# Performance work log

Measured on AMD Instinct MI355X. Metric: run time of the kernel, lower is better.

The kernel has to match this reference:

```python
import jax, jax.numpy as jnp
import numpy as np

N, M, NCAPS, NHID, ROUTIT = 50000, 16, 8, 16, 6
D = NCAPS * NHID  # 128


def _normalize(x, axis):
    # torch fn.normalize: x / max(||x||, eps)
    return x / jnp.maximum(jnp.linalg.norm(x, axis=axis, keepdims=True), 1e-12)


def _routing(x, nb, k, dd, max_iter, fc_w=None, fc_b=None):
    # x: [n, d], nb: [n*m] int indices into rows of x (n == zero pad row)
    if fc_w is not None:
        x = jax.nn.relu(x @ fc_w.T + fc_b)
    n = x.shape[0]
    d = k * dd
    m = nb.shape[0] // n
    xn = _normalize(x.reshape(n, k, dd), 2)          # [n,k,dd]
    zsrc = jnp.concatenate([xn.reshape(n, d), jnp.zeros((1, d), x.dtype)], axis=0)
    z = zsrc[nb].reshape(n, m, k, dd)                # gathered neighbors
    u = xn
    for it in range(max_iter):
        p = jax.nn.softmax(jnp.einsum('nmkd,nkd->nmk', z, u), axis=2)
        u = jnp.einsum('nmkd,nmk->nkd', z, p) + xn
        if it < max_iter - 1:
            u = _normalize(u, 2)
    return u.reshape(n, d)


def setup_inputs() -> dict:
    key = jax.random.key(0)
    k1, k2, k3 = jax.random.split(key, 3)
    x = jax.random.normal(k1, (N, D), dtype=jnp.float32)
    nb = jax.random.randint(k2, (N * M,), 0, N)
    fc1_w = jax.random.normal(k3, (D, D), dtype=jnp.float32) * (1.0 / np.sqrt(D))
    fc1_b = jnp.zeros((D,), dtype=jnp.float32)
    return {"x": x, "nb": nb, "fc1_w": fc1_w, "fc1_b": fc1_b}


def reference(x, nb, fc1_w, fc1_b):
    nb = nb.reshape(-1)
    # layer 0: inp_caps=None -> no fc; dropout is identity in eval mode
    h = jax.nn.relu(_routing(x, nb, NCAPS, NHID, ROUTIT))
    # layer 1: fc Linear(D, D) then relu inside routing
    h = jax.nn.relu(_routing(h, nb, NCAPS, NHID, ROUTIT, fc1_w, fc1_b))
    return h
```

## Files before the change

### kernel.cpp

```cpp
#include <hip/hip_runtime.h>
#include <math.h>

#define N_NODES 50000
#define M_NB 16
#define K_CAPS 8
#define DD 16
#define D_DIM 128
#define ROUTIT 6

template <int CTRL>
__device__ __forceinline__ float dpp_add(float x) {
    int t = __builtin_amdgcn_update_dpp(0, __float_as_int(x), CTRL, 0xF, 0xF, true);
    return x + __int_as_float(t);
}

__device__ __forceinline__ float xor8_add(float x) {
    float d;
    asm("s_nop 1\n\t"
        "v_add_f32_dpp %0, %1, %1 row_ror:8 row_mask:0xf bank_mask:0xf"
        : "=v"(d) : "v"(x));
    return d;
}

__device__ __forceinline__ float xor16_add(float x) {
#if __has_builtin(__builtin_amdgcn_permlane16_swap)
    unsigned xi = __float_as_uint(x);
    auto r = __builtin_amdgcn_permlane16_swap(xi, xi, false, false);
    return __uint_as_float(r[0]) + __uint_as_float(r[1]);
#else
    return x + __int_as_float(__builtin_amdgcn_ds_swizzle(__float_as_int(x), 0x401F));
#endif
}

__device__ __forceinline__ float xor32_add(float x) {
#if __has_builtin(__builtin_amdgcn_permlane32_swap)
    unsigned xi = __float_as_uint(x);
    auto r = __builtin_amdgcn_permlane32_swap(xi, xi, false, false);
    return __uint_as_float(r[0]) + __uint_as_float(r[1]);
#else
    return x + __shfl_xor(x, 32);
#endif
}

__device__ __forceinline__ float fast_rcp(float x) {
#if __has_builtin(__builtin_amdgcn_rcpf)
    return __builtin_amdgcn_rcpf(x);
#else
    return 1.0f / x;
#endif
}

__device__ __forceinline__ float fast_rsq(float x) {
#if __has_builtin(__builtin_amdgcn_rsqf)
    return __builtin_amdgcn_rsqf(x);
#else
    return 1.0f / sqrtf(x);
#endif
}

__device__ __forceinline__ float fast_exp2(float x) {
#if __has_builtin(__builtin_amdgcn_exp2f)
    return __builtin_amdgcn_exp2f(x);
#else
    return __expf(x * 0.6931471805599453f);
#endif
}

__device__ __forceinline__ float2 pk_fma(float2 a, float2 b, float2 c) {
    float2 d;
    asm("v_pk_fma_f32 %0, %1, %2, %3" : "=v"(d) : "v"(a), "v"(b), "v"(c));
    return d;
}

__device__ __forceinline__ float2 bf2(unsigned w) {
    return make_float2(__uint_as_float(w << 16),
                       __uint_as_float(w & 0xFFFF0000u));
}

__device__ __forceinline__ unsigned cvt_pk_bf16(float lo, float hi) {
    unsigned r;
    asm("v_cvt_pk_bf16_f32 %0, %1, %2" : "=v"(r) : "v"(lo), "v"(hi));
    return r;
}

__device__ __forceinline__ unsigned short f2bf(float v) {
    unsigned u = __float_as_uint(v);
    u = (u + 0x7FFFu + ((u >> 16) & 1u)) >> 16;
    return (unsigned short)u;
}

#define BFLY16(CTRLSTR)                                                        \
    asm ("s_nop 1\n\t"                                                         \
         "v_add_f32_dpp %0, %0, %0 "   CTRLSTR "\n\t"                          \
         "v_add_f32_dpp %1, %1, %1 "   CTRLSTR "\n\t"                          \
         "v_add_f32_dpp %2, %2, %2 "   CTRLSTR "\n\t"                          \
         "v_add_f32_dpp %3, %3, %3 "   CTRLSTR "\n\t"                          \
         "v_add_f32_dpp %4, %4, %4 "   CTRLSTR "\n\t"                          \
         "v_add_f32_dpp %5, %5, %5 "   CTRLSTR "\n\t"                          \
         "v_add_f32_dpp %6, %6, %6 "   CTRLSTR "\n\t"                          \
         "v_add_f32_dpp %7, %7, %7 "   CTRLSTR "\n\t"                          \
         "v_add_f32_dpp %8, %8, %8 "   CTRLSTR "\n\t"                          \
         "v_add_f32_dpp %9, %9, %9 "   CTRLSTR "\n\t"                          \
         "v_add_f32_dpp %10, %10, %10 " CTRLSTR "\n\t"                         \
         "v_add_f32_dpp %11, %11, %11 " CTRLSTR "\n\t"                         \
         "v_add_f32_dpp %12, %12, %12 " CTRLSTR "\n\t"                         \
         "v_add_f32_dpp %13, %13, %13 " CTRLSTR "\n\t"                         \
         "v_add_f32_dpp %14, %14, %14 " CTRLSTR "\n\t"                         \
         "v_add_f32_dpp %15, %15, %15 " CTRLSTR                                \
         : "+v"(u[0].x), "+v"(u[0].y), "+v"(u[1].x), "+v"(u[1].y),             \
           "+v"(u[2].x), "+v"(u[2].y), "+v"(u[3].x), "+v"(u[3].y),             \
           "+v"(u[4].x), "+v"(u[4].y), "+v"(u[5].x), "+v"(u[5].y),             \
           "+v"(u[6].x), "+v"(u[6].y), "+v"(u[7].x), "+v"(u[7].y))

__global__ void normalize_kernel(const float* __restrict__ x,
                                 unsigned short* __restrict__ xnb) {
    int tid = blockIdx.x * blockDim.x + threadIdx.x;
    if (tid >= N_NODES * K_CAPS) return;
    const float4* p = reinterpret_cast<const float4*>(x + (size_t)tid * DD);
    float4 a0 = p[0], a1 = p[1], a2 = p[2], a3 = p[3];
    float s = a0.x*a0.x + a0.y*a0.y + a0.z*a0.z + a0.w*a0.w
            + a1.x*a1.x + a1.y*a1.y + a1.z*a1.z + a1.w*a1.w
            + a2.x*a2.x + a2.y*a2.y + a2.z*a2.z + a2.w*a2.w
            + a3.x*a3.x + a3.y*a3.y + a3.z*a3.z + a3.w*a3.w;
    float inv = 1.0f / fmaxf(sqrtf(s), 1e-12f);
    a0.x *= inv; a0.y *= inv; a0.z *= inv; a0.w *= inv;
    a1.x *= inv; a1.y *= inv; a1.z *= inv; a1.w *= inv;
    a2.x *= inv; a2.y *= inv; a2.z *= inv; a2.w *= inv;
    a3.x *= inv; a3.y *= inv; a3.z *= inv; a3.w *= inv;
    uint4 w0, w1;
    w0.x = cvt_pk_bf16(a0.x, a0.y); w0.y = cvt_pk_bf16(a0.z, a0.w);
    w0.z = cvt_pk_bf16(a1.x, a1.y); w0.w = cvt_pk_bf16(a1.z, a1.w);
    w1.x = cvt_pk_bf16(a2.x, a2.y); w1.y = cvt_pk_bf16(a2.z, a2.w);
    w1.z = cvt_pk_bf16(a3.x, a3.y); w1.w = cvt_pk_bf16(a3.z, a3.w);
    uint4* q = reinterpret_cast<uint4*>(xnb + (size_t)tid * DD);
    q[0] = w0; q[1] = w1;
}

__global__ __launch_bounds__(256)
void routing_kernel(const unsigned short* __restrict__ xnb,
                    const int* __restrict__ nb,
                    float* __restrict__ out) {
    const int wave = threadIdx.x >> 6;
    const int lane = threadIdx.x & 63;
    const int node = blockIdx.x * 4 + wave;
    const int mh = lane & 7;
    const int k  = lane >> 3;

    const int idx0 = nb[node * M_NB + mh];
    const int idx1 = nb[node * M_NB + mh + 8];
    const uint4* zp0 = reinterpret_cast<const uint4*>(xnb + (size_t)idx0 * D_DIM + k * DD);
    const uint4* zp1 = reinterpret_cast<const uint4*>(xnb + (size_t)idx1 * D_DIM + k * DD);
    uint4 A0 = zp0[0], A1 = zp0[1];
    uint4 B0 = zp1[0], B1 = zp1[1];

    const uint4* xp = reinterpret_cast<const uint4*>(xnb + (size_t)node * D_DIM + k * DD);
    uint4 X0 = xp[0], X1 = xp[1];

    float2 z0[8], z1[8], u[8], xs[8];
    z0[0] = bf2(A0.x); z0[1] = bf2(A0.y); z0[2] = bf2(A0.z); z0[3] = bf2(A0.w);
    z0[4] = bf2(A1.x); z0[5] = bf2(A1.y); z0[6] = bf2(A1.z); z0[7] = bf2(A1.w);
    z1[0] = bf2(B0.x); z1[1] = bf2(B0.y); z1[2] = bf2(B0.z); z1[3] = bf2(B0.w);
    z1[4] = bf2(B1.x); z1[5] = bf2(B1.y); z1[6] = bf2(B1.z); z1[7] = bf2(B1.w);
    u[0] = bf2(X0.x); u[1] = bf2(X0.y); u[2] = bf2(X0.z); u[3] = bf2(X0.w);
    u[4] = bf2(X1.x); u[5] = bf2(X1.y); u[6] = bf2(X1.z); u[7] = bf2(X1.w);
#pragma unroll
    for (int j = 0; j < 8; ++j)
        xs[j] = make_float2(u[j].x * 0.125f, u[j].y * 0.125f);

    const float LOG2E = 1.4426950408889634f;
    const float2 zero2 = make_float2(0.f, 0.f);
    float s2 = LOG2E;

#pragma unroll
    for (int it = 0; it < ROUTIT; ++it) {
        float2 a0 = pk_fma(z0[0], u[0], zero2);
        float2 a1 = pk_fma(z0[1], u[1], zero2);
        a0 = pk_fma(z0[2], u[2], a0);
        a1 = pk_fma(z0[3], u[3], a1);
        a0 = pk_fma(z0[4], u[4], a0);
        a1 = pk_fma(z0[5], u[5], a1);
        a0 = pk_fma(z0[6], u[6], a0);
        a1 = pk_fma(z0[7], u[7], a1);
        float2 b0 = pk_fma(z1[0], u[0], zero2);
        float2 b1 = pk_fma(z1[1], u[1], zero2);
        b0 = pk_fma(z1[2], u[2], b0);
        b1 = pk_fma(z1[3], u[3], b1);
        b0 = pk_fma(z1[4], u[4], b0);
        b1 = pk_fma(z1[5], u[5], b1);
        b0 = pk_fma(z1[6], u[6], b0);
        b1 = pk_fma(z1[7], u[7], b1);
        float l0 = (a0.x + a0.y) + (a1.x + a1.y);
        float l1 = (b0.x + b0.y) + (b1.x + b1.y);

        float e0 = fast_exp2(l0 * s2);
        float e1 = fast_exp2(l1 * s2);
        float t0 = xor8_add(e0);  float t1 = xor8_add(e1);
        t0 = xor16_add(t0);       t1 = xor16_add(t1);
        t0 = xor32_add(t0);       t1 = xor32_add(t1);
        float p0 = e0 * fast_rcp(t0);
        float p1 = e1 * fast_rcp(t1);

        float2 p0b = make_float2(p0, p0);
        float2 p1b = make_float2(p1, p1);
#pragma unroll
        for (int j = 0; j < 8; ++j)
            u[j] = pk_fma(z1[j], p1b, pk_fma(z0[j], p0b, xs[j]));

        BFLY16("quad_perm:[1,0,3,2] row_mask:0xf bank_mask:0xf");
        BFLY16("quad_perm:[2,3,0,1] row_mask:0xf bank_mask:0xf");
        BFLY16("row_half_mirror row_mask:0xf bank_mask:0xf");

        if (it < ROUTIT - 1) {
            float2 q0 = pk_fma(u[0], u[0], zero2);
            float2 q1 = pk_fma(u[1], u[1], zero2);
            q0 = pk_fma(u[2], u[2], q0);
            q1 = pk_fma(u[3], u[3], q1);
            q0 = pk_fma(u[4], u[4], q0);
            q1 = pk_fma(u[5], u[5], q1);
            q0 = pk_fma(u[6], u[6], q0);
            q1 = pk_fma(u[7], u[7], q1);
            float nrm = (q0.x + q0.y) + (q1.x + q1.y);
            s2 = fast_rsq(fmaxf(nrm, 1e-24f)) * LOG2E;
        }
    }

#pragma unroll
    for (int j = 0; j < 8; ++j) {
        u[j].x = fmaxf(u[j].x, 0.f);
        u[j].y = fmaxf(u[j].y, 0.f);
    }
#pragma unroll
    for (int j = 0; j < 4; ++j) {
        if (mh == j) {
            float4 v = make_float4(u[2*j].x, u[2*j].y, u[2*j+1].x, u[2*j+1].y);
            *reinterpret_cast<float4*>(out + (size_t)node * D_DIM + k * DD + j * 4) = v;
        }
    }
}

__global__ __launch_bounds__(256, 2)
void fc_norm_kernel(const float* __restrict__ h,
                    const float* __restrict__ W,
                    const float* __restrict__ b,
                    unsigned short* __restrict__ xnbout) {
    __shared__ float4 Wt4[32 * 129];
    __shared__ float4 hrow4[8 * 32];

    const float4* W4 = reinterpret_cast<const float4*>(W);
    for (int t = threadIdx.x; t < 128 * 32; t += 256) {
        Wt4[(t & 31) * 129 + (t >> 5)] = W4[t];
    }
    __syncthreads();

    const int col = threadIdx.x & 127;
    const int rr  = threadIdx.x >> 7;
    const float bias = b[col];

    for (int row0 = blockIdx.x * 8; row0 < N_NODES; row0 += gridDim.x * 8) {
        __syncthreads();
        {
            int t = threadIdx.x;
            hrow4[t] = *reinterpret_cast<const float4*>(
                h + (size_t)(row0 + (t >> 5)) * D_DIM + (t & 31) * 4);
        }
        __syncthreads();

        float acc0 = bias, acc1 = bias, acc2 = bias, acc3 = bias;
#pragma unroll
        for (int k4 = 0; k4 < 32; ++k4) {
            float4 w4 = Wt4[k4 * 129 + col];
            float4 h0 = hrow4[(rr * 4 + 0) * 32 + k4];
            float4 h1 = hrow4[(rr * 4 + 1) * 32 + k4];
            float4 h2 = hrow4[(rr * 4 + 2) * 32 + k4];
            float4 h3 = hrow4[(rr * 4 + 3) * 32 + k4];
            acc0 = fmaf(w4.x, h0.x, acc0); acc0 = fmaf(w4.y, h0.y, acc0);
            acc0 = fmaf(w4.z, h0.z, acc0); acc0 = fmaf(w4.w, h0.w, acc0);
            acc1 = fmaf(w4.x, h1.x, acc1); acc1 = fmaf(w4.y, h1.y, acc1);
            acc1 = fmaf(w4.z, h1.z, acc1); acc1 = fmaf(w4.w, h1.w, acc1);
            acc2 = fmaf(w4.x, h2.x, acc2); acc2 = fmaf(w4.y, h2.y, acc2);
            acc2 = fmaf(w4.z, h2.z, acc2); acc2 = fmaf(w4.w, h2.w, acc2);
            acc3 = fmaf(w4.x, h3.x, acc3); acc3 = fmaf(w4.y, h3.y, acc3);
            acc3 = fmaf(w4.z, h3.z, acc3); acc3 = fmaf(w4.w, h3.w, acc3);
        }

        float a[4] = {fmaxf(acc0, 0.f), fmaxf(acc1, 0.f),
                      fmaxf(acc2, 0.f), fmaxf(acc3, 0.f)};
#pragma unroll
        for (int j = 0; j < 4; ++j) {
            float s = a[j] * a[j];
            s = dpp_add<0xB1>(s);
            s = dpp_add<0x4E>(s);
            s = dpp_add<0x141>(s);
            s = dpp_add<0x140>(s);
            float inv = fast_rsq(fmaxf(s, 1e-24f));
            xnbout[(size_t)(row0 + rr * 4 + j) * D_DIM + col] = f2bf(a[j] * inv);
        }
    }
}

extern "C" void kernel_launch(void* const* d_in, const int* in_sizes, int n_in,
                              void* d_out, int out_size, void* d_ws, size_t ws_size,
                              hipStream_t stream) {
    const float* x  = (const float*)d_in[0];
    const int*   nb = (const int*)d_in[1];
    const float* W  = (const float*)d_in[2];
    const float* bb = (const float*)d_in[3];
    float* out = (float*)d_out;

    unsigned short* xnb = (unsigned short*)d_ws;
    float* h0 = (float*)((char*)d_ws + (size_t)N_NODES * D_DIM * 2);

    normalize_kernel<<<(N_NODES * K_CAPS + 255) / 256, 256, 0, stream>>>(x, xnb);
    routing_kernel<<<N_NODES / 4, 256, 0, stream>>>(xnb, nb, h0);
    fc_norm_kernel<<<1024, 256, 0, stream>>>(h0, W, bb, xnb);
    routing_kernel<<<N_NODES / 4, 256, 0, stream>>>(xnb, nb, out);
}
```

Measured before the change: 205.1 us.

## Make routing kernel persistent with software-prefetched neighbor gathers

The routing kernel becomes a grid-stride persistent kernel launched with 1024 blocks, where each wave handles many nodes. While it computes the current node, it issues the gather loads for the next node and the index loads for the one after. The aim is to hide the latency of the random neighbor gathers behind the routing arithmetic and to cut block launch overhead. In exchange, more registers stay live for the prefetched data, which may lower occupancy, and the fixed grid size may leave compute units unevenly loaded.

```diff
diff --git a/kernel.cpp b/kernel.cpp
--- a/kernel.cpp
+++ b/kernel.cpp
@@ -136,26 +136,9 @@
     q[0] = w0; q[1] = w1;
 }
 
-__global__ __launch_bounds__(256)
-void routing_kernel(const unsigned short* __restrict__ xnb,
-                    const int* __restrict__ nb,
-                    float* __restrict__ out) {
-    const int wave = threadIdx.x >> 6;
-    const int lane = threadIdx.x & 63;
-    const int node = blockIdx.x * 4 + wave;
-    const int mh = lane & 7;
-    const int k  = lane >> 3;
-
-    const int idx0 = nb[node * M_NB + mh];
-    const int idx1 = nb[node * M_NB + mh + 8];
-    const uint4* zp0 = reinterpret_cast<const uint4*>(xnb + (size_t)idx0 * D_DIM + k * DD);
-    const uint4* zp1 = reinterpret_cast<const uint4*>(xnb + (size_t)idx1 * D_DIM + k * DD);
-    uint4 A0 = zp0[0], A1 = zp0[1];
-    uint4 B0 = zp1[0], B1 = zp1[1];
-
-    const uint4* xp = reinterpret_cast<const uint4*>(xnb + (size_t)node * D_DIM + k * DD);
-    uint4 X0 = xp[0], X1 = xp[1];
-
+__device__ __forceinline__ void route_node(
+        uint4 A0, uint4 A1, uint4 B0, uint4 B1, uint4 X0, uint4 X1,
+        int node, int mh, int k, float* __restrict__ out) {
     float2 z0[8], z1[8], u[8], xs[8];
     z0[0] = bf2(A0.x); z0[1] = bf2(A0.y); z0[2] = bf2(A0.z); z0[3] = bf2(A0.w);
     z0[4] = bf2(A1.x); z0[5] = bf2(A1.y); z0[6] = bf2(A1.z); z0[7] = bf2(A1.w);
@@ -238,6 +221,60 @@
     }
 }
 
+__global__ __launch_bounds__(256)
+void routing_kernel(const unsigned short* __restrict__ xnb,
+                    const int* __restrict__ nb,
+                    float* __restrict__ out) {
+    const int wave = threadIdx.x >> 6;
+    const int lane = threadIdx.x & 63;
+    const int wid  = blockIdx.x * 4 + wave;
+    const int NW   = gridDim.x * 4;
+    const int mh = lane & 7;
+    const int k  = lane >> 3;
+    const size_t koff = (size_t)k * DD;
+
+    int node = wid;
+    if (node >= N_NODES) return;
+
+    int i0 = nb[node * M_NB + mh];
+    int i1 = nb[node * M_NB + mh + 8];
+    const uint4* zp0 = reinterpret_cast<const uint4*>(xnb + (size_t)i0 * D_DIM + koff);
+    const uint4* zp1 = reinterpret_cast<const uint4*>(xnb + (size_t)i1 * D_DIM + koff);
+    const uint4* xp  = reinterpret_cast<const uint4*>(xnb + (size_t)node * D_DIM + koff);
+    uint4 A0 = zp0[0], A1 = zp0[1];
+    uint4 B0 = zp1[0], B1 = zp1[1];
+    uint4 X0 = xp[0],  X1 = xp[1];
+
+    int node1 = node + NW;
+    int j0 = 0, j1 = 0;
+    if (node1 < N_NODES) {
+        j0 = nb[node1 * M_NB + mh];
+        j1 = nb[node1 * M_NB + mh + 8];
+    }
+
+    while (true) {
+        const bool have_next = (node1 < N_NODES);
+        uint4 nA0, nA1, nB0, nB1, nX0, nX1;
+        if (have_next) {
+            const uint4* nzp0 = reinterpret_cast<const uint4*>(xnb + (size_t)j0 * D_DIM + koff);
+            const uint4* nzp1 = reinterpret_cast<const uint4*>(xnb + (size_t)j1 * D_DIM + koff);
+            const uint4* nxp  = reinterpret_cast<const uint4*>(xnb + (size_t)node1 * D_DIM + koff);
+            nA0 = nzp0[0]; nA1 = nzp0[1];
+            nB0 = nzp1[0]; nB1 = nzp1[1];
+            nX0 = nxp[0];  nX1 = nxp[1];
+            int node2 = node1 + NW;
+            if (node2 < N_NODES) {
+                j0 = nb[node2 * M_NB + mh];
+                j1 = nb[node2 * M_NB + mh + 8];
+            }
+        }
+        route_node(A0, A1, B0, B1, X0, X1, node, mh, k, out);
+        if (!have_next) break;
+        A0 = nA0; A1 = nA1; B0 = nB0; B1 = nB1; X0 = nX0; X1 = nX1;
+        node = node1; node1 = node1 + NW;
+    }
+}
+
 __global__ __launch_bounds__(256, 2)
 void fc_norm_kernel(const float* __restrict__ h,
                     const float* __restrict__ W,
@@ -311,7 +348,7 @@
     float* h0 = (float*)((char*)d_ws + (size_t)N_NODES * D_DIM * 2);
 
     normalize_kernel<<<(N_NODES * K_CAPS + 255) / 256, 256, 0, stream>>>(x, xnb);
-    routing_kernel<<<N_NODES / 4, 256, 0, stream>>>(xnb, nb, h0);
+    routing_kernel<<<1024, 256, 0, stream>>>(xnb, nb, h0);
     fc_norm_kernel<<<1024, 256, 0, stream>>>(h0, W, bb, xnb);
-    routing_kernel<<<N_NODES / 4, 256, 0, stream>>>(xnb, nb, out);
-}
+    routing_kernel<<<1024, 256, 0, stream>>>(xnb, nb, out);
+}
```

New measurement: 239.3 us. 1.17x slower.
